# Performance work log

Hardware: AMD Instinct MI355X
Metric: run time of the kernel (lower is better)

## Reference

```python
import jax, jax.numpy as jnp
import numpy as np

GROUP_SIZE = 64
OUT_F, IN_F = 11008, 4096
W_SHAPE = (OUT_F, IN_F)


def quantize_q40(w):
    # w: fp32 weight, numel divisible by GROUP_SIZE
    wg = w.reshape(-1, GROUP_SIZE)                      # [N, G]
    wmax = jnp.max(jnp.abs(wg), axis=1)
    scale = (wmax / 7.0).astype(jnp.float16)[:, None]   # [N, 1] fp16 per-group scale
    quant = wg / scale.astype(jnp.float32)
    q = jnp.round(quant).astype(jnp.int8)               # values in [-7, 7]
    pairs = q.reshape(-1, 2, GROUP_SIZE)                # even rows -> MSB nibble, odd -> LSB
    packed = ((pairs[:, 0] << 4) | (pairs[:, 1] & 15)).astype(jnp.int8)  # [N/2, G]
    return packed, scale


def dequantize_q40(w, scale):
    # w: int8 packed [N/2, G]; arithmetic shifts sign-extend each nibble
    msb = w >> 4
    lsb = (w << 4) >> 4
    full = jnp.concatenate([msb, lsb], axis=1).reshape(-1, GROUP_SIZE)  # interleave back to [N, G]
    return (full.astype(jnp.float16) * scale).reshape(W_SHAPE)


def setup_inputs() -> dict:
    key = jax.random.key(0)
    kx, kw = jax.random.split(key)
    x = jax.random.normal(kx, (4, 2048, IN_F), dtype=jnp.float16)
    w_fp = jax.random.normal(kw, W_SHAPE, dtype=jnp.float32) * 0.02
    linear_w, linear_s = quantize_q40(w_fp)
    return {"x": x, "linear_w": linear_w, "linear_s": linear_s}


def reference(x, linear_w, linear_s):
    # dequantize packed int4 weights to fp16, then dense linear (no bias)
    deq = dequantize_q40(linear_w, linear_s)            # [OUT_F, IN_F] fp16
    return jnp.einsum('bsi,oi->bso', x, deq)            # F.linear(x, deq)
```

## Files before the change

kernel.cpp:

```cpp
#include <hip/hip_runtime.h>
#include <stdint.h>

#define IN_F   4096
#define OUT_F  11008
#define M_ROWS 8192
#define BM 256
#define BN 256
#define BK 64
#define NTILE_K (IN_F / BK)

typedef __attribute__((ext_vector_type(4))) float  f32x4;
typedef __attribute__((ext_vector_type(4))) int    int4v;
typedef __attribute__((ext_vector_type(8))) unsigned short ushort8;
typedef __bf16 bf16x8 __attribute__((ext_vector_type(8)));

__device__ __forceinline__ unsigned short f2bf(float f) {
  unsigned int u = __builtin_bit_cast(unsigned int, f);
  u += 0x7fffu + ((u >> 16) & 1u);
  return (unsigned short)(u >> 16);
}

__global__ __launch_bounds__(256) void dequant_q40(const int* __restrict__ w,
                                                   const float* __restrict__ sc,
                                                   unsigned short* __restrict__ wb) {
  const int total8 = (OUT_F * IN_F) / 8;
  for (int t = blockIdx.x * blockDim.x + threadIdx.x; t < total8;
       t += gridDim.x * blockDim.x) {
    const int f0  = t * 8;
    const int p   = f0 >> 7;
    const int nib = (f0 >> 6) & 1;
    const int j0  = f0 & 63;
    const float scale = sc[f0 >> 6];
    const int* src = w + p * 64 + j0;
    const int4v b0 = __builtin_nontemporal_load(reinterpret_cast<const int4v*>(src));
    const int4v b1 = __builtin_nontemporal_load(reinterpret_cast<const int4v*>(src + 4));
    ushort8 r;
#pragma unroll
    for (int e = 0; e < 4; ++e) {
      const int v0 = b0[e], v1 = b1[e];
      const int q0 = nib ? ((v0 << 28) >> 28) : (v0 >> 4);
      const int q1 = nib ? ((v1 << 28) >> 28) : (v1 >> 4);
      r[e]     = f2bf((float)q0 * scale);
      r[4 + e] = f2bf((float)q1 * scale);
    }
    *reinterpret_cast<ushort8*>(wb + f0) = r;
  }
}

__global__ __launch_bounds__(256) void cvt_x(const float* __restrict__ x,
                                             unsigned short* __restrict__ xb) {
  const int total8 = (M_ROWS * IN_F) / 8;
  for (int t = blockIdx.x * blockDim.x + threadIdx.x; t < total8;
       t += gridDim.x * blockDim.x) {
    const f32x4 a0 = __builtin_nontemporal_load(reinterpret_cast<const f32x4*>(x + t * 8));
    const f32x4 a1 = __builtin_nontemporal_load(reinterpret_cast<const f32x4*>(x + t * 8 + 4));
    ushort8 r;
#pragma unroll
    for (int e = 0; e < 4; ++e) {
      r[e]     = f2bf(a0[e]);
      r[4 + e] = f2bf(a1[e]);
    }
    *reinterpret_cast<ushort8*>(xb + t * 8) = r;
  }
}

__device__ __forceinline__ void gld16(const void* g, void* l) {
  __builtin_amdgcn_global_load_lds(
      (const __attribute__((address_space(1))) unsigned int*)(uintptr_t)g,
      (__attribute__((address_space(3))) unsigned int*)(unsigned int)(uintptr_t)l,
      16, 0, 0);
}

#define BAR() do { asm volatile("" ::: "memory"); __builtin_amdgcn_s_barrier(); \
                   asm volatile("" ::: "memory"); } while (0)

__global__ __launch_bounds__(512, 2) void gemm_bt(const unsigned short* __restrict__ A,
                                                  const unsigned short* __restrict__ B,
                                                  float* __restrict__ C) {
  __shared__ __align__(16) unsigned short lds[65536];

  const int NT  = OUT_F / BN;
  const int nwg = (M_ROWS / BM) * NT;
  const int cpx = nwg >> 3;
  const int bid = blockIdx.x;
  const int swz = (bid & 7) * cpx + (bid >> 3);
  const int mt  = swz / NT;
  const int nt  = swz - mt * NT;

  const int tid  = threadIdx.x;
  const int lane = tid & 63;
  const int wid  = tid >> 6;
  const int wr   = wid >> 2;
  const int wc   = wid & 3;

  const int r_st = tid >> 2;
  const int lc   = (tid & 3) ^ ((tid >> 3) & 3);
  const unsigned short* gA = A + (size_t)(mt * BM + r_st) * IN_F + lc * 8;
  const unsigned short* gB = B + (size_t)(nt * BM + r_st) * IN_F + lc * 8;
  unsigned short* ldsw = lds + tid * 8;

#define STAGE_A(b, h, kk) do {                                              \
    unsigned short* d_ = ldsw + (b) * 32768 + (h) * 8192;                   \
    const unsigned short* s_ = gA + (kk) + (h) * 32;                        \
    gld16(s_, d_); gld16(s_ + (size_t)128 * IN_F, d_ + 4096);               \
  } while (0)
#define STAGE_B(b, h, kk) do {                                              \
    unsigned short* d_ = ldsw + (b) * 32768 + 16384 + (h) * 8192;           \
    const unsigned short* s_ = gB + (kk) + (h) * 32;                        \
    gld16(s_, d_); gld16(s_ + (size_t)128 * IN_F, d_ + 4096);               \
  } while (0)

  const int fr   = lane & 15;
  const int kq   = lane >> 4;
  const int coff = (kq ^ ((fr >> 1) & 3)) * 8;

  bf16x8 aS0[4], aS1[4], bS0[4], bS1[4];
#define RD_A(dst, b, h, mq) do {                                            \
    const unsigned short* p_ = lds + (b) * 32768 + (h) * 8192 + coff;       \
    _Pragma("unroll") for (int mm = 0; mm < 4; ++mm)                        \
      dst[mm] = *reinterpret_cast<const bf16x8*>(                           \
          p_ + (size_t)(wr * 128 + (mq) * 64 + mm * 16 + fr) * 32);         \
  } while (0)
#define RD_B(dst, b, h) do {                                                \
    const unsigned short* p_ = lds + (b) * 32768 + 16384 + (h) * 8192 + coff; \
    _Pragma("unroll") for (int nn = 0; nn < 4; ++nn)                        \
      dst[nn] = *reinterpret_cast<const bf16x8*>(                           \
          p_ + (size_t)(wc * 64 + nn * 16 + fr) * 32);                      \
  } while (0)

  f32x4 acc[8][4] = {};
#define MFMA16(mq, aset, bset) do {                                         \
    __builtin_amdgcn_s_setprio(1);                                          \
    _Pragma("unroll") for (int mm = 0; mm < 4; ++mm)                        \
      _Pragma("unroll") for (int nn = 0; nn < 4; ++nn)                      \
        acc[(mq)*4+mm][nn] = __builtin_amdgcn_mfma_f32_16x16x32_bf16(       \
            aset[mm], bset[nn], acc[(mq)*4+mm][nn], 0, 0, 0);               \
    __builtin_amdgcn_s_setprio(0);                                          \
  } while (0)

#define VWAIT6() asm volatile("s_waitcnt vmcnt(6)" ::: "memory")

  STAGE_A(0, 0, 0); STAGE_B(0, 0, 0);
  STAGE_A(0, 1, 0); STAGE_B(0, 1, 0);
  STAGE_A(1, 0, BK); STAGE_B(1, 0, BK);
  asm volatile("s_waitcnt vmcnt(8)" ::: "memory");
  BAR();
  RD_A(aS0, 0, 0, 0); RD_B(bS0, 0, 0);

  for (int it = 0; it < NTILE_K / 2; ++it) {
    const int kt1 = ((2 * it + 1) & (NTILE_K - 1)) * BK;
    const int kt2 = ((2 * it + 2) & (NTILE_K - 1)) * BK;
    const int kt3 = ((2 * it + 3) & (NTILE_K - 1)) * BK;

    STAGE_A(1, 1, kt1); RD_A(aS1, 0, 0, 1); VWAIT6();
    BAR(); MFMA16(0, aS0, bS0);
    STAGE_B(1, 1, kt1); RD_A(aS0, 0, 1, 0); RD_B(bS1, 0, 1);
    BAR(); MFMA16(1, aS1, bS0);
    STAGE_A(0, 0, kt2); RD_A(aS1, 0, 1, 1); VWAIT6();
    BAR(); MFMA16(0, aS0, bS1);
    STAGE_B(0, 0, kt2); RD_A(aS0, 1, 0, 0); RD_B(bS0, 1, 0);
    BAR(); MFMA16(1, aS1, bS1);
    STAGE_A(0, 1, kt2); RD_A(aS1, 1, 0, 1); VWAIT6();
    BAR(); MFMA16(0, aS0, bS0);
    STAGE_B(0, 1, kt2); RD_A(aS0, 1, 1, 0); RD_B(bS1, 1, 1);
    BAR(); MFMA16(1, aS1, bS0);
    STAGE_A(1, 0, kt3); RD_A(aS1, 1, 1, 1); VWAIT6();
    BAR(); MFMA16(0, aS0, bS1);
    STAGE_B(1, 0, kt3); RD_A(aS0, 0, 0, 0); RD_B(bS0, 0, 0);
    BAR(); MFMA16(1, aS1, bS1);
  }

  const int col  = nt * BN + wc * 64 + fr;
  const int row0 = mt * BM + wr * 128 + (lane >> 4) * 4;
#pragma unroll
  for (int m = 0; m < 8; ++m) {
#pragma unroll
    for (int n = 0; n < 4; ++n) {
      float* cp = C + (size_t)(row0 + m * 16) * OUT_F + (col + n * 16);
#pragma unroll
      for (int r = 0; r < 4; ++r) cp[(size_t)r * OUT_F] = acc[m][n][r];
    }
  }
}

extern "C" void kernel_launch(void* const* d_in, const int* in_sizes, int n_in,
                              void* d_out, int out_size, void* d_ws, size_t ws_size,
                              hipStream_t stream) {
  const float* x = (const float*)d_in[0];
  const int*   w = (const int*)d_in[1];
  const float* s = (const float*)d_in[2];
  float*     out = (float*)d_out;

  unsigned short* wb = (unsigned short*)d_ws;
  unsigned short* xb = wb + (size_t)OUT_F * IN_F;

  dequant_q40<<<dim3(2048), dim3(256), 0, stream>>>(w, s, wb);
  cvt_x<<<dim3(2048), dim3(256), 0, stream>>>(x, xb);
  gemm_bt<<<dim3((M_ROWS / BM) * (OUT_F / BN)), dim3(512), 0, stream>>>(xb, wb, out);
}
```

Before: 745.3 us.

## Shrink GEMM M-tile to 128 and simplify the LDS double-buffer pipeline

Halves the GEMM block tile along M from 256 to 128. Each wave now holds a 4x4 accumulator set instead of 8x4, and LDS shrinks to 96KB. The K-loop is rewritten as four steps per iteration, each staging A and B together with a uniform vmcnt wait, replacing the interleaved half-tile schedule. The aim is to cut register and LDS pressure and improve wave-quantization balance across CUs, at the cost of less data reuse per loaded B tile and more B traffic from global memory.

```diff
diff --git a/kernel.cpp b/kernel.cpp
--- a/kernel.cpp
+++ b/kernel.cpp
@@ -4,7 +4,7 @@
 #define IN_F   4096
 #define OUT_F  11008
 #define M_ROWS 8192
-#define BM 256
+#define BM 128
 #define BN 256
 #define BK 64
 #define NTILE_K (IN_F / BK)
@@ -77,7 +77,7 @@
 __global__ __launch_bounds__(512, 2) void gemm_bt(const unsigned short* __restrict__ A,
                                                   const unsigned short* __restrict__ B,
                                                   float* __restrict__ C) {
-  __shared__ __align__(16) unsigned short lds[65536];
+  __shared__ __align__(16) unsigned short lds[49152];
 
   const int NT  = OUT_F / BN;
   const int nwg = (M_ROWS / BM) * NT;
@@ -96,16 +96,14 @@
   const int r_st = tid >> 2;
   const int lc   = (tid & 3) ^ ((tid >> 3) & 3);
   const unsigned short* gA = A + (size_t)(mt * BM + r_st) * IN_F + lc * 8;
-  const unsigned short* gB = B + (size_t)(nt * BM + r_st) * IN_F + lc * 8;
+  const unsigned short* gB = B + (size_t)(nt * BN + r_st) * IN_F + lc * 8;
   unsigned short* ldsw = lds + tid * 8;
 
 #define STAGE_A(b, h, kk) do {                                              \
-    unsigned short* d_ = ldsw + (b) * 32768 + (h) * 8192;                   \
-    const unsigned short* s_ = gA + (kk) + (h) * 32;                        \
-    gld16(s_, d_); gld16(s_ + (size_t)128 * IN_F, d_ + 4096);               \
+    gld16(gA + (kk) + (h) * 32, ldsw + (b) * 24576 + (h) * 4096);           \
   } while (0)
 #define STAGE_B(b, h, kk) do {                                              \
-    unsigned short* d_ = ldsw + (b) * 32768 + 16384 + (h) * 8192;           \
+    unsigned short* d_ = ldsw + (b) * 24576 + 8192 + (h) * 8192;            \
     const unsigned short* s_ = gB + (kk) + (h) * 32;                        \
     gld16(s_, d_); gld16(s_ + (size_t)128 * IN_F, d_ + 4096);               \
   } while (0)
@@ -115,65 +113,65 @@
   const int coff = (kq ^ ((fr >> 1) & 3)) * 8;
 
   bf16x8 aS0[4], aS1[4], bS0[4], bS1[4];
-#define RD_A(dst, b, h, mq) do {                                            \
-    const unsigned short* p_ = lds + (b) * 32768 + (h) * 8192 + coff;       \
+#define RD_A(dst, b, h) do {                                                \
+    const unsigned short* p_ = lds + (b) * 24576 + (h) * 4096 + coff;       \
     _Pragma("unroll") for (int mm = 0; mm < 4; ++mm)                        \
       dst[mm] = *reinterpret_cast<const bf16x8*>(                           \
-          p_ + (size_t)(wr * 128 + (mq) * 64 + mm * 16 + fr) * 32);         \
+          p_ + (size_t)(wr * 64 + mm * 16 + fr) * 32);                      \
   } while (0)
 #define RD_B(dst, b, h) do {                                                \
-    const unsigned short* p_ = lds + (b) * 32768 + 16384 + (h) * 8192 + coff; \
+    const unsigned short* p_ = lds + (b) * 24576 + 8192 + (h) * 8192 + coff; \
     _Pragma("unroll") for (int nn = 0; nn < 4; ++nn)                        \
       dst[nn] = *reinterpret_cast<const bf16x8*>(                           \
           p_ + (size_t)(wc * 64 + nn * 16 + fr) * 32);                      \
   } while (0)
 
-  f32x4 acc[8][4] = {};
-#define MFMA16(mq, aset, bset) do {                                         \
+  f32x4 acc[4][4] = {};
+#define MFMA16(aset, bset) do {                                             \
     __builtin_amdgcn_s_setprio(1);                                          \
     _Pragma("unroll") for (int mm = 0; mm < 4; ++mm)                        \
       _Pragma("unroll") for (int nn = 0; nn < 4; ++nn)                      \
-        acc[(mq)*4+mm][nn] = __builtin_amdgcn_mfma_f32_16x16x32_bf16(       \
-            aset[mm], bset[nn], acc[(mq)*4+mm][nn], 0, 0, 0);               \
+        acc[mm][nn] = __builtin_amdgcn_mfma_f32_16x16x32_bf16(              \
+            aset[mm], bset[nn], acc[mm][nn], 0, 0, 0);                      \
     __builtin_amdgcn_s_setprio(0);                                          \
   } while (0)
 
 #define VWAIT6() asm volatile("s_waitcnt vmcnt(6)" ::: "memory")
 
-  STAGE_A(0, 0, 0); STAGE_B(0, 0, 0);
-  STAGE_A(0, 1, 0); STAGE_B(0, 1, 0);
+  STAGE_A(0, 0, 0);  STAGE_B(0, 0, 0);
+  STAGE_A(0, 1, 0);  STAGE_B(0, 1, 0);
   STAGE_A(1, 0, BK); STAGE_B(1, 0, BK);
-  asm volatile("s_waitcnt vmcnt(8)" ::: "memory");
+  STAGE_A(1, 1, BK); STAGE_B(1, 1, BK);
+  VWAIT6();
   BAR();
-  RD_A(aS0, 0, 0, 0); RD_B(bS0, 0, 0);
+  RD_A(aS0, 0, 0); RD_B(bS0, 0, 0);
 
   for (int it = 0; it < NTILE_K / 2; ++it) {
-    const int kt1 = ((2 * it + 1) & (NTILE_K - 1)) * BK;
     const int kt2 = ((2 * it + 2) & (NTILE_K - 1)) * BK;
     const int kt3 = ((2 * it + 3) & (NTILE_K - 1)) * BK;
 
-    STAGE_A(1, 1, kt1); RD_A(aS1, 0, 0, 1); VWAIT6();
-    BAR(); MFMA16(0, aS0, bS0);
-    STAGE_B(1, 1, kt1); RD_A(aS0, 0, 1, 0); RD_B(bS1, 0, 1);
-    BAR(); MFMA16(1, aS1, bS0);
-    STAGE_A(0, 0, kt2); RD_A(aS1, 0, 1, 1); VWAIT6();
-    BAR(); MFMA16(0, aS0, bS1);
-    STAGE_B(0, 0, kt2); RD_A(aS0, 1, 0, 0); RD_B(bS0, 1, 0);
-    BAR(); MFMA16(1, aS1, bS1);
-    STAGE_A(0, 1, kt2); RD_A(aS1, 1, 0, 1); VWAIT6();
-    BAR(); MFMA16(0, aS0, bS0);
-    STAGE_B(0, 1, kt2); RD_A(aS0, 1, 1, 0); RD_B(bS1, 1, 1);
-    BAR(); MFMA16(1, aS1, bS0);
-    STAGE_A(1, 0, kt3); RD_A(aS1, 1, 1, 1); VWAIT6();
-    BAR(); MFMA16(0, aS0, bS1);
-    STAGE_B(1, 0, kt3); RD_A(aS0, 0, 0, 0); RD_B(bS0, 0, 0);
-    BAR(); MFMA16(1, aS1, bS1);
+    STAGE_A(0, 0, kt2); STAGE_B(0, 0, kt2);
+    RD_A(aS1, 0, 1); RD_B(bS1, 0, 1);
+    VWAIT6();
+    BAR(); MFMA16(aS0, bS0);
+    STAGE_A(0, 1, kt2); STAGE_B(0, 1, kt2);
+    RD_A(aS0, 1, 0); RD_B(bS0, 1, 0);
+    VWAIT6();
+    BAR(); MFMA16(aS1, bS1);
+    STAGE_A(1, 0, kt3); STAGE_B(1, 0, kt3);
+    RD_A(aS1, 1, 1); RD_B(bS1, 1, 1);
+    VWAIT6();
+    BAR(); MFMA16(aS0, bS0);
+    STAGE_A(1, 1, kt3); STAGE_B(1, 1, kt3);
+    RD_A(aS0, 0, 0); RD_B(bS0, 0, 0);
+    VWAIT6();
+    BAR(); MFMA16(aS1, bS1);
   }
 
   const int col  = nt * BN + wc * 64 + fr;
-  const int row0 = mt * BM + wr * 128 + (lane >> 4) * 4;
+  const int row0 = mt * BM + wr * 64 + (lane >> 4) * 4;
 #pragma unroll
-  for (int m = 0; m < 8; ++m) {
+  for (int m = 0; m < 4; ++m) {
 #pragma unroll
     for (int n = 0; n < 4; ++n) {
       float* cp = C + (size_t)(row0 + m * 16) * OUT_F + (col + n * 16);
```

New measurement: 1.003 ms. 34.6% more time.

## Fuse int4 weight dequantization into GEMM B-tile loads from LDS

Applied to the files above, without the earlier changes.

Instead of dequantizing the full weight matrix to bf16 in a separate pass, the weights are repacked into a dense 4-bit row-major layout and the scales are transposed to fp16. The GEMM then stages packed nibbles and scales into LDS and dequantizes them to bf16 in registers while building the B fragments. This cuts global traffic for the weight operand and removes the large bf16 weight write and read. In exchange it adds ALU work for unpacking and conversion inside the MFMA loop, plus a new pipeline schedule and barrier layout that could stall the matrix units.

```diff
diff --git a/kernel.cpp b/kernel.cpp
--- a/kernel.cpp
+++ b/kernel.cpp
@@ -20,30 +20,38 @@
   return (unsigned short)(u >> 16);
 }
 
-__global__ __launch_bounds__(256) void dequant_q40(const int* __restrict__ w,
-                                                   const float* __restrict__ sc,
-                                                   unsigned short* __restrict__ wb) {
-  const int total8 = (OUT_F * IN_F) / 8;
-  for (int t = blockIdx.x * blockDim.x + threadIdx.x; t < total8;
-       t += gridDim.x * blockDim.x) {
-    const int f0  = t * 8;
-    const int p   = f0 >> 7;
-    const int nib = (f0 >> 6) & 1;
-    const int j0  = f0 & 63;
-    const float scale = sc[f0 >> 6];
+__global__ __launch_bounds__(256) void pack_w(const int* __restrict__ w,
+                                              unsigned int* __restrict__ wq) {
+  const int totald = OUT_F * (IN_F / 8);
+  for (int d = blockIdx.x * blockDim.x + threadIdx.x; d < totald;
+       d += gridDim.x * blockDim.x) {
+    const int o   = d >> 9;
+    const int k0  = (d & 511) * 8;
+    const int n   = o * 64 + (k0 >> 6);
+    const int p   = n >> 1;
+    const int nib = n & 1;
+    const int j0  = k0 & 63;
     const int* src = w + p * 64 + j0;
     const int4v b0 = __builtin_nontemporal_load(reinterpret_cast<const int4v*>(src));
     const int4v b1 = __builtin_nontemporal_load(reinterpret_cast<const int4v*>(src + 4));
-    ushort8 r;
-#pragma unroll
-    for (int e = 0; e < 4; ++e) {
-      const int v0 = b0[e], v1 = b1[e];
-      const int q0 = nib ? ((v0 << 28) >> 28) : (v0 >> 4);
-      const int q1 = nib ? ((v1 << 28) >> 28) : (v1 >> 4);
-      r[e]     = f2bf((float)q0 * scale);
-      r[4 + e] = f2bf((float)q1 * scale);
+    unsigned int acc = 0;
+#pragma unroll
+    for (int i = 0; i < 8; ++i) {
+      const int b = (i < 4) ? b0[i] : b1[i - 4];
+      const int q = nib ? ((b << 28) >> 28) : (b >> 4);
+      acc |= ((unsigned int)(q & 0xF)) << (4 * i);
     }
-    *reinterpret_cast<ushort8*>(wb + f0) = r;
+    wq[d] = acc;
+  }
+}
+
+__global__ __launch_bounds__(256) void scale_t(const float* __restrict__ s,
+                                               unsigned short* __restrict__ st) {
+  const int o = blockIdx.x * 256 + threadIdx.x;
+  const int g = blockIdx.y;
+  if (o < OUT_F) {
+    _Float16 h = (_Float16)s[o * 64 + g];
+    st[g * OUT_F + o] = __builtin_bit_cast(unsigned short, h);
   }
 }
 
@@ -75,9 +83,10 @@
                    asm volatile("" ::: "memory"); } while (0)
 
 __global__ __launch_bounds__(512, 2) void gemm_bt(const unsigned short* __restrict__ A,
-                                                  const unsigned short* __restrict__ B,
+                                                  const unsigned char* __restrict__ WQ,
+                                                  const unsigned short* __restrict__ ST,
                                                   float* __restrict__ C) {
-  __shared__ __align__(16) unsigned short lds[65536];
+  __shared__ __align__(16) unsigned short lds[57344];
 
   const int NT  = OUT_F / BN;
   const int nwg = (M_ROWS / BM) * NT;
@@ -86,6 +95,7 @@
   const int swz = (bid & 7) * cpx + (bid >> 3);
   const int mt  = swz / NT;
   const int nt  = swz - mt * NT;
+  const int n0  = nt * BN;
 
   const int tid  = threadIdx.x;
   const int lane = tid & 63;
@@ -96,18 +106,22 @@
   const int r_st = tid >> 2;
   const int lc   = (tid & 3) ^ ((tid >> 3) & 3);
   const unsigned short* gA = A + (size_t)(mt * BM + r_st) * IN_F + lc * 8;
-  const unsigned short* gB = B + (size_t)(nt * BM + r_st) * IN_F + lc * 8;
   unsigned short* ldsw = lds + tid * 8;
 
 #define STAGE_A(b, h, kk) do {                                              \
-    unsigned short* d_ = ldsw + (b) * 32768 + (h) * 8192;                   \
+    unsigned short* d_ = ldsw + (b) * 16384 + (h) * 8192;                   \
     const unsigned short* s_ = gA + (kk) + (h) * 32;                        \
     gld16(s_, d_); gld16(s_ + (size_t)128 * IN_F, d_ + 4096);               \
   } while (0)
-#define STAGE_B(b, h, kk) do {                                              \
-    unsigned short* d_ = ldsw + (b) * 32768 + 16384 + (h) * 8192;           \
-    const unsigned short* s_ = gB + (kk) + (h) * 32;                        \
-    gld16(s_, d_); gld16(s_ + (size_t)128 * IN_F, d_ + 4096);               \
+
+  const unsigned char* gBQ = WQ + (size_t)(n0 + (tid >> 1)) * (IN_F / 2) + (tid & 1) * 16;
+#define STAGE_BQ(b, tk) \
+    gld16(gBQ + (tk) * 32, lds + 32768 + (b) * 4096 + tid * 8)
+
+#define STAGE_SL(c) do {                                                    \
+    const int sl_ = (c) * 512 + tid;                                        \
+    gld16(ST + (size_t)(sl_ >> 5) * OUT_F + n0 + (sl_ & 31) * 8,            \
+          lds + 40960 + sl_ * 8);                                           \
   } while (0)
 
   const int fr   = lane & 15;
@@ -116,16 +130,24 @@
 
   bf16x8 aS0[4], aS1[4], bS0[4], bS1[4];
 #define RD_A(dst, b, h, mq) do {                                            \
-    const unsigned short* p_ = lds + (b) * 32768 + (h) * 8192 + coff;       \
+    const unsigned short* p_ = lds + (b) * 16384 + (h) * 8192 + coff;       \
     _Pragma("unroll") for (int mm = 0; mm < 4; ++mm)                        \
       dst[mm] = *reinterpret_cast<const bf16x8*>(                           \
           p_ + (size_t)(wr * 128 + (mq) * 64 + mm * 16 + fr) * 32);         \
   } while (0)
-#define RD_B(dst, b, h) do {                                                \
-    const unsigned short* p_ = lds + (b) * 32768 + 16384 + (h) * 8192 + coff; \
-    _Pragma("unroll") for (int nn = 0; nn < 4; ++nn)                        \
-      dst[nn] = *reinterpret_cast<const bf16x8*>(                           \
-          p_ + (size_t)(wc * 64 + nn * 16 + fr) * 32);                      \
+
+#define RD_B(dst, b, h, g) do {                                             \
+    _Pragma("unroll") for (int nn = 0; nn < 4; ++nn) {                      \
+      const int o_ = wc * 64 + nn * 16 + fr;                                \
+      const unsigned int w4 = *reinterpret_cast<const unsigned int*>(       \
+          lds + 32768 + (b) * 4096 + o_ * 16 + ((h) * 4 + kq) * 2);         \
+      const float sc_ = (float)(*reinterpret_cast<const _Float16*>(         \
+          lds + 40960 + (g) * 256 + o_));                                   \
+      _Pragma("unroll") for (int i = 0; i < 8; ++i) {                       \
+        const int v_ = ((int)(w4 << (28 - 4 * i))) >> 28;                   \
+        dst[nn][i] = (__bf16)((float)v_ * sc_);                             \
+      }                                                                     \
+    }                                                                       \
   } while (0)
 
   f32x4 acc[8][4] = {};
@@ -138,39 +160,47 @@
     __builtin_amdgcn_s_setprio(0);                                          \
   } while (0)
 
-#define VWAIT6() asm volatile("s_waitcnt vmcnt(6)" ::: "memory")
-
-  STAGE_A(0, 0, 0); STAGE_B(0, 0, 0);
-  STAGE_A(0, 1, 0); STAGE_B(0, 1, 0);
-  STAGE_A(1, 0, BK); STAGE_B(1, 0, BK);
-  asm volatile("s_waitcnt vmcnt(8)" ::: "memory");
+#define VW(n) asm volatile("s_waitcnt vmcnt(" #n ")" ::: "memory")
+
+  STAGE_SL(0); STAGE_SL(1); STAGE_SL(2); STAGE_SL(3);
+  STAGE_BQ(0, 0);
+  STAGE_A(0, 0, 0);
+  STAGE_A(0, 1, 0);
+  STAGE_A(1, 0, BK);
+  VW(4);
   BAR();
-  RD_A(aS0, 0, 0, 0); RD_B(bS0, 0, 0);
+  RD_A(aS0, 0, 0, 0); RD_B(bS0, 0, 0, 0);
 
   for (int it = 0; it < NTILE_K / 2; ++it) {
-    const int kt1 = ((2 * it + 1) & (NTILE_K - 1)) * BK;
-    const int kt2 = ((2 * it + 2) & (NTILE_K - 1)) * BK;
-    const int kt3 = ((2 * it + 3) & (NTILE_K - 1)) * BK;
-
-    STAGE_A(1, 1, kt1); RD_A(aS1, 0, 0, 1); VWAIT6();
+    const int t1i = 2 * it + 1;
+    const int t2i = (2 * it + 2) & (NTILE_K - 1);
+    const int t3i = (2 * it + 3) & (NTILE_K - 1);
+    const int kt1 = t1i * BK, kt2 = t2i * BK, kt3 = t3i * BK;
+
+    STAGE_BQ(1, t1i); STAGE_A(1, 1, kt1);
+    RD_A(aS1, 0, 0, 1); VW(5);
     BAR(); MFMA16(0, aS0, bS0);
-    STAGE_B(1, 1, kt1); RD_A(aS0, 0, 1, 0); RD_B(bS1, 0, 1);
+    RD_A(aS0, 0, 1, 0); RD_B(bS1, 0, 1, 2 * it);
     BAR(); MFMA16(1, aS1, bS0);
-    STAGE_A(0, 0, kt2); RD_A(aS1, 0, 1, 1); VWAIT6();
+    STAGE_A(0, 0, kt2);
+    RD_A(aS1, 0, 1, 1); VW(4);
     BAR(); MFMA16(0, aS0, bS1);
-    STAGE_B(0, 0, kt2); RD_A(aS0, 1, 0, 0); RD_B(bS0, 1, 0);
+    STAGE_BQ(0, t2i);
+    RD_A(aS0, 1, 0, 0); RD_B(bS0, 1, 0, t1i);
     BAR(); MFMA16(1, aS1, bS1);
-    STAGE_A(0, 1, kt2); RD_A(aS1, 1, 0, 1); VWAIT6();
+    STAGE_A(0, 1, kt2);
+    RD_A(aS1, 1, 0, 1); VW(5);
     BAR(); MFMA16(0, aS0, bS0);
-    STAGE_B(0, 1, kt2); RD_A(aS0, 1, 1, 0); RD_B(bS1, 1, 1);
+    RD_A(aS0, 1, 1, 0); RD_B(bS1, 1, 1, t1i);
     BAR(); MFMA16(1, aS1, bS0);
-    STAGE_A(1, 0, kt3); RD_A(aS1, 1, 1, 1); VWAIT6();
+    STAGE_A(1, 0, kt3);
+    RD_A(aS1, 1, 1, 1); VW(4);
     BAR(); MFMA16(0, aS0, bS1);
-    STAGE_B(1, 0, kt3); RD_A(aS0, 0, 0, 0); RD_B(bS0, 0, 0);
+    RD_A(aS0, 0, 0, 0); RD_B(bS0, 0, 0, t2i);
     BAR(); MFMA16(1, aS1, bS1);
   }
 
-  const int col  = nt * BN + wc * 64 + fr;
+  const int col  = n0 + wc * 64 + fr;
   const int row0 = mt * BM + wr * 128 + (lane >> 4) * 4;
 #pragma unroll
   for (int m = 0; m < 8; ++m) {
@@ -191,10 +221,12 @@
   const float* s = (const float*)d_in[2];
   float*     out = (float*)d_out;
 
-  unsigned short* wb = (unsigned short*)d_ws;
-  unsigned short* xb = wb + (size_t)OUT_F * IN_F;
-
-  dequant_q40<<<dim3(2048), dim3(256), 0, stream>>>(w, s, wb);
+  unsigned short* xb = (unsigned short*)d_ws;
+  unsigned char*  wq = (unsigned char*)d_ws + (size_t)M_ROWS * IN_F * 2;
+  unsigned short* st = (unsigned short*)(wq + (size_t)OUT_F * (IN_F / 2));
+
+  pack_w<<<dim3(2048), dim3(256), 0, stream>>>(w, (unsigned int*)wq);
+  scale_t<<<dim3(43, 64), dim3(256), 0, stream>>>(s, st);
   cvt_x<<<dim3(2048), dim3(256), 0, stream>>>(x, xb);
-  gemm_bt<<<dim3((M_ROWS / BM) * (OUT_F / BN)), dim3(512), 0, stream>>>(xb, wb, out);
-}
+  gemm_bt<<<dim3((M_ROWS / BM) * (OUT_F / BN)), dim3(512), 0, stream>>>(xb, wq, st, out);
+}
```

Result: slower. 1.522 ms (+104.2%).
